# Optimization experiments

Measured on AMD Instinct MI355X. Metric: run time of the kernel, lower is better.

Reference implementation:

```python
import jax, jax.numpy as jnp
import numpy as np

B, T, V, E, H = 32, 128, 32000, 512, 1024
START = 1


def setup_inputs() -> dict:
    key = jax.random.key(0)
    ks = jax.random.split(key, 16)
    s = 0.02
    inp = {
        'h0': jax.random.normal(ks[0], (B, H), jnp.float32),
        'c0': jax.random.normal(ks[1], (B, H), jnp.float32),
        'h1': jax.random.normal(ks[2], (B, H), jnp.float32),
        'c1': jax.random.normal(ks[3], (B, H), jnp.float32),
        'h2': jax.random.normal(ks[4], (B, H), jnp.float32),
        'c2': jax.random.normal(ks[5], (B, H), jnp.float32),
        'h3': jax.random.normal(ks[6], (B, H), jnp.float32),
        'c3': jax.random.normal(ks[7], (B, H), jnp.float32),
        'emb': jax.random.normal(ks[8], (V, E), jnp.float32) * s,
        'Wx0': jax.random.normal(ks[9], (E, 4 * H), jnp.float32) * s,
        'Wh0': jax.random.normal(ks[10], (H, 4 * H), jnp.float32) * s,
        'b0': jnp.zeros((4 * H,), jnp.float32),
        'Wx1': jax.random.normal(ks[11], (H, 4 * H), jnp.float32) * s,
        'Wh1': jax.random.normal(ks[12], (H, 4 * H), jnp.float32) * s,
        'b1': jnp.zeros((4 * H,), jnp.float32),
        'Wx2': jax.random.normal(ks[13], (H, 4 * H), jnp.float32) * s,
        'Wh2': jax.random.normal(ks[14], (H, 4 * H), jnp.float32) * s,
        'b2': jnp.zeros((4 * H,), jnp.float32),
        'Wx3': jax.random.normal(ks[15], (H, 4 * H), jnp.float32) * s,
        'Wh3': jax.random.normal(jax.random.fold_in(key, 99), (H, 4 * H), jnp.float32) * s,
        'b3': jnp.zeros((4 * H,), jnp.float32),
        'fcW': jax.random.normal(jax.random.fold_in(key, 100), (H, V), jnp.float32) * s,
        'fcb': jnp.zeros((V,), jnp.float32),
        'target_length': T,
    }
    return inp


def _lstm_cell(x, h, c, Wx, Wh, b):
    # Keras gate order: i, f, c(candidate), o
    z = x @ Wx + h @ Wh + b  # [B, 4H]
    i, f, g, o = jnp.split(z, 4, axis=-1)
    i = jax.nn.sigmoid(i)
    f = jax.nn.sigmoid(f)
    g = jnp.tanh(g)
    o = jax.nn.sigmoid(o)
    c_new = f * c + i * g
    h_new = o * jnp.tanh(c_new)
    return h_new, c_new


def reference(h0, c0, h1, c1, h2, c2, h3, c3, emb,
              Wx0, Wh0, b0, Wx1, Wh1, b1, Wx2, Wh2, b2, Wx3, Wh3, b3,
              fcW, fcb, target_length):
    n_batch = h0.shape[0]
    tok0 = jnp.full((n_batch,), START, dtype=jnp.int32)

    def step(carry, _):
        tok, h0, c0, h1, c1, h2, c2, h3, c3 = carry
        x = emb[tok]  # [B, E]
        h0, c0 = _lstm_cell(x, h0, c0, Wx0, Wh0, b0)
        h1, c1 = _lstm_cell(h0, h1, c1, Wx1, Wh1, b1)
        h2, c2 = _lstm_cell(h1, h2, c2, Wx2, Wh2, b2)
        h3, c3 = _lstm_cell(h2, h3, c3, Wx3, Wh3, b3)
        logits = h3 @ fcW + fcb  # [B, V]
        tok = jnp.argmax(logits, axis=1).astype(jnp.int32)
        return (tok, h0, c0, h1, c1, h2, c2, h3, c3), (logits, tok)

    carry0 = (tok0, h0, c0, h1, c1, h2, c2, h3, c3)
    _, (logits_seq, ids_seq) = jax.lax.scan(step, carry0, None, length=target_length)
    outputs_prob = jnp.transpose(logits_seq, (1, 0, 2))  # [B, T, V]
    outputs = jnp.transpose(ids_seq, (1, 0))             # [B, T]
    return outputs_prob, outputs
```

## Files before the change

kernel.cpp:

```cpp
#include <hip/hip_runtime.h>
#include <stdint.h>

#define NBLK 256
#define NTHR 1024

typedef _Float16 f16;
typedef _Float16 f16x8 __attribute__((ext_vector_type(8)));
typedef float f32x4 __attribute__((ext_vector_type(4)));
typedef unsigned long long u64;


__device__ __forceinline__ void split2(float w, f16& hi, f16& lo) {
  f16 h = (__builtin_fabsf(w) < 6.104e-05f) ? (f16)0.0f : (f16)w;
  hi = h;
  lo = (f16)((w - (float)h) * 2048.0f);
}

__device__ __forceinline__ void split3(float w, f16& h, f16& l, f16& m) {
  const float hf = (__builtin_fabsf(w) < 6.104e-05f) ? 0.0f : (float)(f16)w;
  h = (f16)hf;
  const float r1s = (w - hf) * 2048.0f;
  const float lf = (__builtin_fabsf(r1s) < 6.104e-05f) ? 0.0f : (float)(f16)r1s;
  l = (f16)lf;
  const float r2s = (r1s - lf) * 2048.0f;
  m = (__builtin_fabsf(r2s) < 6.104e-05f) ? (f16)0.0f : (f16)r2s;
}

__device__ __forceinline__ float sig32(float z) {
  const float e32 = (float)exp(-(double)z);
  return 1.0f / __fadd_rn(1.0f, e32);
}
__device__ __forceinline__ float tanh32f(float z) { return (float)tanh((double)z); }

__device__ __forceinline__ u64 packvc(float v, unsigned col) {
  unsigned u = __float_as_uint(v);
  u = (u & 0x80000000u) ? ~u : (u | 0x80000000u);
  return ((u64)u << 32) | (u64)(0xFFFFFFFFu - col);
}
__device__ __forceinline__ u64 umax64(u64 a, u64 b) { return a > b ? a : b; }

__device__ __forceinline__ size_t faddr(int k, int row) {
  return (size_t)(((k >> 5) * 2 + (row >> 4)) * 512 +
                  (16 * ((k >> 3) & 3) + (row & 15)) * 8 + (k & 7));
}


struct MainP {
  const float* emb;
  const float* bias[4];
  const float* fcb;
  const float* hini[4];
  const float* cini[4];
  const f16* WfH[4];
  const f16* WfL[4];
  const f16* fcH;
  const f16* fcLc;
  const float* shat;
  f16* axh[5];
  f16* axl[5];
  f16* axm[5];
  u64* top;
  unsigned* bar;
  float* out;
};


__device__ __forceinline__ void grid_bar2(unsigned* bar, int blk) {
  __syncthreads();
  if (threadIdx.x == 0) {
    const int g = blk >> 5;
    unsigned* gcnt = bar + g * 32;
    unsigned* ggen = bar + g * 32 + 16;
    unsigned* tcnt = bar + 512;
    unsigned* tgen = bar + 528;
    unsigned gg = __hip_atomic_load(ggen, __ATOMIC_RELAXED, __HIP_MEMORY_SCOPE_AGENT);
    unsigned prev = __hip_atomic_fetch_add(gcnt, 1u, __ATOMIC_ACQ_REL, __HIP_MEMORY_SCOPE_AGENT);
    if (prev == 31u) {
      unsigned tg = __hip_atomic_load(tgen, __ATOMIC_RELAXED, __HIP_MEMORY_SCOPE_AGENT);
      unsigned p2 = __hip_atomic_fetch_add(tcnt, 1u, __ATOMIC_ACQ_REL, __HIP_MEMORY_SCOPE_AGENT);
      if (p2 == 7u) {
        __hip_atomic_store(tcnt, 0u, __ATOMIC_RELAXED, __HIP_MEMORY_SCOPE_AGENT);
        __hip_atomic_store(tgen, tg + 1u, __ATOMIC_RELEASE, __HIP_MEMORY_SCOPE_AGENT);
      } else {
        while (__hip_atomic_load(tgen, __ATOMIC_RELAXED, __HIP_MEMORY_SCOPE_AGENT) == tg)
          __builtin_amdgcn_s_sleep(1);
        __builtin_amdgcn_fence(__ATOMIC_ACQUIRE, "agent");
      }
      __hip_atomic_store(gcnt, 0u, __ATOMIC_RELAXED, __HIP_MEMORY_SCOPE_AGENT);
      __hip_atomic_store(ggen, gg + 1u, __ATOMIC_RELEASE, __HIP_MEMORY_SCOPE_AGENT);
    } else {
      while (__hip_atomic_load(ggen, __ATOMIC_RELAXED, __HIP_MEMORY_SCOPE_AGENT) == gg)
        __builtin_amdgcn_s_sleep(2);
      __builtin_amdgcn_fence(__ATOMIC_ACQUIRE, "agent");
    }
  }
  __syncthreads();
}


__global__ __launch_bounds__(256) void prep_lstm(const float* Wx, const float* Wh,
                                                 int Kx, int CH, f16* dh, f16* dl) {
  const int id = blockIdx.x * 256 + threadIdx.x;
  const int lane = id & 63;
  const int cw = id >> 6;
  const int tile = cw / CH;
  if (tile >= 256) return;
  const int chunk = cw - tile * CH;
  const int n16 = lane & 15, qq = lane >> 4;
  const int col = 1024 * (n16 >> 2) + 4 * tile + (n16 & 3);
  const int kb = chunk * 32 + 8 * qq;
  f16x8 hv, lv;
#pragma unroll
  for (int e = 0; e < 8; ++e) {
    const int k = kb + e;
    const float wv = (k < Kx) ? Wx[(size_t)k * 4096 + col] : Wh[(size_t)(k - Kx) * 4096 + col];
    f16 h, l;
    split2(wv, h, l);
    hv[e] = h; lv[e] = l;
  }
  const size_t d = ((size_t)cw * 64 + lane) * 8;
  *(f16x8*)(dh + d) = hv;
  *(f16x8*)(dl + d) = lv;
}

__global__ __launch_bounds__(256) void prep_fc(const float* fcW, f16* dh) {
  const int id = blockIdx.x * 256 + threadIdx.x;
  const int lane = id & 63;
  const int cw = id >> 6;
  const int chunk = cw & 31;
  const int stb = cw >> 5;
  const int st = stb & 7, blk = stb >> 3;
  if (blk >= 256) return;
  const int n16 = lane & 15, qq = lane >> 4;
  int cl = st * 16 + n16;
  if (cl > 124) cl = 124;
  const int col = 125 * blk + cl;
  const int kb = chunk * 32 + 8 * qq;
  f16x8 hv;
#pragma unroll
  for (int e = 0; e < 8; ++e) {
    const float wv = fcW[(size_t)(kb + e) * 32000 + col];
    f16 h, l;
    split2(wv, h, l);
    hv[e] = h; (void)l;
  }
  const size_t d = ((size_t)cw * 64 + lane) * 8;
  *(f16x8*)(dh + d) = hv;
}

__global__ __launch_bounds__(256) void prep_fclT(const float* fcW, f16* fcLc) {
  const int col0 = blockIdx.x * 64;
  const int tid = threadIdx.x;
  __shared__ float lds[64][65];
  for (int pass = 0; pass < 16; ++pass) {
    const int kbase = pass * 64;
#pragma unroll
    for (int rr = 0; rr < 16; ++rr) {
      const int kk = rr * 4 + (tid >> 6);
      lds[kk][tid & 63] = fcW[(size_t)(kbase + kk) * 32000 + col0 + (tid & 63)];
    }
    __syncthreads();
    {
      const int col = tid >> 2, qr = tid & 3;
      f16x8 v0, v1;
#pragma unroll
      for (int i = 0; i < 8; ++i) {
        f16 h, l;
        split2(lds[qr * 16 + i][col], h, l);
        v0[i] = l;
      }
#pragma unroll
      for (int i = 0; i < 8; ++i) {
        f16 h, l;
        split2(lds[qr * 16 + 8 + i][col], h, l);
        v1[i] = l;
      }
      const size_t d = (size_t)(col0 + col) * 1024 + kbase + qr * 16;
      *(f16x8*)(fcLc + d) = v0;
      *(f16x8*)(fcLc + d + 8) = v1;
    }
    __syncthreads();
  }
}

__global__ __launch_bounds__(256) void prep_shat(const float* fcW, float* shat) {
  const int id = blockIdx.x * 256 + threadIdx.x;
  if (id >= 256 * 1024) return;
  const int blk = id >> 10, k = id & 1023;
  const float* src = fcW + (size_t)k * 32000 + 125 * blk;
  float s = 0.f;
  for (int c = 0; c < 125; ++c) {
    f16 h, l;
    split2(src[c], h, l);
    s = fmaxf(s, __builtin_fabsf((float)l));
  }
  shat[id] = s;
}

__global__ void ws_sentinel(float* out) {
  if (blockIdx.x == 0 && threadIdx.x == 0) out[0] = 1.0e9f;
}


__global__ __launch_bounds__(NTHR, 4) void lstm_main(MainP p) {
  const int blk = blockIdx.x;
  const int tid = threadIdx.x;
  const int lane = tid & 63;
  const int w = tid >> 6;
  const int q = lane >> 4;
  const int n16 = lane & 15;

  __shared__ float zpart[16][2][32][16];
  __shared__ float fcpart[2][32][128];
  __shared__ float zred[32][16];
  __shared__ float rmaxs[32][16];
  __shared__ float epart[32][16];
  __shared__ float rowmax[32];
  __shared__ float erow[32];
  __shared__ float cst[4][32][4];
  __shared__ f16 hs_h[32][4], hs_l[32][4], hs_m[32][4];
  __shared__ int tokS[32];
  __shared__ u64 redu[32][16];
  __shared__ u64 redu2[32];
  __shared__ int wl[4000];
  __shared__ unsigned cand[32][4];
  __shared__ int wcount;

  if (tid < 512) {
    const int i = tid;
    const int l = i >> 7, b = (i >> 2) & 31, j = i & 3;
    cst[l][b][j] = p.cini[l][b * 1024 + 4 * blk + j];
    f16 hh, ll, mm;
    split3(p.hini[l][b * 1024 + 4 * blk + j], hh, ll, mm);
    const int kp = (l == 0) ? (4 * blk + j) : (1024 + 4 * blk + j);
    const size_t a = faddr(kp, b);
    p.axh[l][a] = hh;
    p.axl[l][a] = ll;
    p.axm[l][a] = mm;
  }
  grid_bar2(p.bar, blk);

  auto layer_tail = [&](int l, const float* bias, f16* dh, f16* dl, f16* dm) {
    __syncthreads();
    if (tid < 512) {
      const int row = tid >> 4, c = tid & 15;
      double A = 0.0, B = 0.0;
#pragma unroll
      for (int w2 = 0; w2 < 16; ++w2) {
        A += (double)zpart[w2][0][row][c];
        B += (double)zpart[w2][1][row][c];
      }
      zred[row][c] = __fadd_rn(__fadd_rn((float)A, (float)B),
                               bias[1024 * (c >> 2) + 4 * blk + (c & 3)]);
    }
    __syncthreads();
    if (tid < 128) {
      const int b = tid >> 2, j = tid & 3;
      const float zi = zred[b][j], zf = zred[b][4 + j], zg = zred[b][8 + j], zo = zred[b][12 + j];
      const float i_ = sig32(zi);
      const float f_ = sig32(zf);
      const float g_ = tanh32f(zg);
      const float o_ = sig32(zo);
      const float c_ = __fadd_rn(__fmul_rn(f_, cst[l][b][j]), __fmul_rn(i_, g_));
      cst[l][b][j] = c_;
      const float h_ = __fmul_rn(o_, tanh32f(c_));
      f16 hh, ll, mm;
      split3(h_, hh, ll, mm);
      hs_h[b][j] = hh; hs_l[b][j] = ll; hs_m[b][j] = mm;
      const size_t a = faddr(4 * blk + j, b);
      dh[a] = hh; dl[a] = ll; dm[a] = mm;
    }
  };

  for (int t = 0; t < 128; ++t) {
    if (t == 0) {
      if (tid < 32) tokS[tid] = 1;
    } else {
      if (tid < 512) {
        const int row = tid >> 4, seg = tid & 15;
        const u64* tr = p.top + row * 256 + seg * 16;
        u64 m = 0;
#pragma unroll
        for (int e = 0; e < 16; ++e) m = umax64(m, tr[e]);
        redu[row][seg] = m;
      }
      __syncthreads();
      if (tid < 32) {
        u64 mm = redu[tid][0];
#pragma unroll
        for (int s2 = 1; s2 < 16; ++s2) mm = umax64(mm, redu[tid][s2]);
        const int tok = (int)(0xFFFFFFFFu - (unsigned)(mm & 0xFFFFFFFFull));
        tokS[tid] = tok;
        if (blk == tid)
          p.out[(size_t)32 * 128 * 32000 + (size_t)tid * 128 + (t - 1)] = (float)tok;
      }
    }
    __syncthreads();

    {
      double zdA0[4] = {0,0,0,0}, zdA1[4] = {0,0,0,0};
      double zdB0[4] = {0,0,0,0}, zdB1[4] = {0,0,0,0};
      const f32x4 zz = {0.f, 0.f, 0.f, 0.f};
      f16x8 WB[6];
#pragma unroll
      for (int sl = 0; sl < 3; ++sl) {
        const size_t wo = ((size_t)(blk * 48 + w * 3 + sl) * 64 + lane) * 8;
        WB[sl * 2] = *(const f16x8*)(p.WfH[0] + wo);
        WB[sl * 2 + 1] = *(const f16x8*)(p.WfL[0] + wo);
      }
#pragma unroll
      for (int sl = 0; sl < 3; ++sl) {
        const int chunk = w * 3 + sl;
        const int k0 = chunk * 32 + 8 * q;
        const f16x8 bh = WB[sl * 2];
        const f16x8 bl = WB[sl * 2 + 1];
        f16x8 ah0, al0, am0, ah1, al1, am1;
        if (chunk < 16) {
          {
            const float* ep = p.emb + (size_t)tokS[n16] * 512 + k0;
            const float4 v0 = *(const float4*)ep;
            const float4 v1 = *(const float4*)(ep + 4);
            const float vv[8] = {v0.x, v0.y, v0.z, v0.w, v1.x, v1.y, v1.z, v1.w};
#pragma unroll
            for (int e = 0; e < 8; ++e) { f16 a,b,c; split3(vv[e],a,b,c); ah0[e]=a; al0[e]=b; am0[e]=c; }
          }
          {
            const float* ep = p.emb + (size_t)tokS[16 + n16] * 512 + k0;
            const float4 v0 = *(const float4*)ep;
            const float4 v1 = *(const float4*)(ep + 4);
            const float vv[8] = {v0.x, v0.y, v0.z, v0.w, v1.x, v1.y, v1.z, v1.w};
#pragma unroll
            for (int e = 0; e < 8; ++e) { f16 a,b,c; split3(vv[e],a,b,c); ah1[e]=a; al1[e]=b; am1[e]=c; }
          }
        } else {
          const int cs = chunk - 16;
          const size_t b0 = (size_t)(cs * 2) * 512 + lane * 8;
          ah0 = *(const f16x8*)(p.axh[0] + b0);
          al0 = *(const f16x8*)(p.axl[0] + b0);
          am0 = *(const f16x8*)(p.axm[0] + b0);
          ah1 = *(const f16x8*)(p.axh[0] + b0 + 512);
          al1 = *(const f16x8*)(p.axl[0] + b0 + 512);
          am1 = *(const f16x8*)(p.axm[0] + b0 + 512);
        }
        f32x4 t00 = __builtin_amdgcn_mfma_f32_16x16x32_f16(ah0, bh, zz, 0, 0, 0);
        f32x4 t10 = __builtin_amdgcn_mfma_f32_16x16x32_f16(ah0, bl, zz, 0, 0, 0);
        t10 = __builtin_amdgcn_mfma_f32_16x16x32_f16(al0, bh, t10, 0, 0, 0);
        f32x4 t20 = __builtin_amdgcn_mfma_f32_16x16x32_f16(al0, bl, zz, 0, 0, 0);
        t20 = __builtin_amdgcn_mfma_f32_16x16x32_f16(am0, bh, t20, 0, 0, 0);
        f32x4 t01 = __builtin_amdgcn_mfma_f32_16x16x32_f16(ah1, bh, zz, 0, 0, 0);
        f32x4 t11 = __builtin_amdgcn_mfma_f32_16x16x32_f16(ah1, bl, zz, 0, 0, 0);
        t11 = __builtin_amdgcn_mfma_f32_16x16x32_f16(al1, bh, t11, 0, 0, 0);
        f32x4 t21 = __builtin_amdgcn_mfma_f32_16x16x32_f16(al1, bl, zz, 0, 0, 0);
        t21 = __builtin_amdgcn_mfma_f32_16x16x32_f16(am1, bh, t21, 0, 0, 0);
        if (chunk < 16) {
#pragma unroll
          for (int r = 0; r < 4; ++r) {
            zdA0[r] += (double)t00[r] + (double)t10[r] * 0x1p-11 + (double)t20[r] * 0x1p-22;
            zdA1[r] += (double)t01[r] + (double)t11[r] * 0x1p-11 + (double)t21[r] * 0x1p-22;
          }
        } else {
#pragma unroll
          for (int r = 0; r < 4; ++r) {
            zdB0[r] += (double)t00[r] + (double)t10[r] * 0x1p-11 + (double)t20[r] * 0x1p-22;
            zdB1[r] += (double)t01[r] + (double)t11[r] * 0x1p-11 + (double)t21[r] * 0x1p-22;
          }
        }
      }
#pragma unroll
      for (int r = 0; r < 4; ++r) {
        zpart[w][0][4 * q + r][n16] = (float)zdA0[r];
        zpart[w][0][16 + 4 * q + r][n16] = (float)zdA1[r];
        zpart[w][1][4 * q + r][n16] = (float)zdB0[r];
        zpart[w][1][16 + 4 * q + r][n16] = (float)zdB1[r];
      }
    }
    layer_tail(0, p.bias[0], p.axh[1], p.axl[1], p.axm[1]);
    grid_bar2(p.bar, blk);

    for (int l = 1; l < 4; ++l) {
      if (tid < 128) {
        const int b = tid >> 2, j = tid & 3;
        const int kp = (l == 1) ? (4 * blk + j) : (1024 + 4 * blk + j);
        const size_t a = faddr(kp, b);
        p.axh[l - 1][a] = hs_h[b][j];
        p.axl[l - 1][a] = hs_l[b][j];
        p.axm[l - 1][a] = hs_m[b][j];
      }
      {
        double zdA0[4] = {0,0,0,0}, zdA1[4] = {0,0,0,0};
        double zdB0[4] = {0,0,0,0}, zdB1[4] = {0,0,0,0};
        const f16* WH = p.WfH[l];
        const f16* WL = p.WfL[l];
        const f16* axh_ = p.axh[l];
        const f16* axl_ = p.axl[l];
        const f16* axm_ = p.axm[l];
        const f32x4 zz = {0.f, 0.f, 0.f, 0.f};
        f16x8 WB[8];
#pragma unroll
        for (int sl = 0; sl < 4; ++sl) {
          const size_t wo = ((size_t)(blk * 64 + w * 4 + sl) * 64 + lane) * 8;
          WB[sl * 2] = *(const f16x8*)(WH + wo);
          WB[sl * 2 + 1] = *(const f16x8*)(WL + wo);
        }
#pragma unroll
        for (int sl = 0; sl < 4; ++sl) {
          const int chunk = w * 4 + sl;
          const f16x8 bh = WB[sl * 2];
          const f16x8 bl = WB[sl * 2 + 1];
          const size_t b0 = (size_t)(chunk * 2) * 512 + lane * 8;
          const f16x8 ah0 = *(const f16x8*)(axh_ + b0);
          const f16x8 al0 = *(const f16x8*)(axl_ + b0);
          const f16x8 am0 = *(const f16x8*)(axm_ + b0);
          const f16x8 ah1 = *(const f16x8*)(axh_ + b0 + 512);
          const f16x8 al1 = *(const f16x8*)(axl_ + b0 + 512);
          const f16x8 am1 = *(const f16x8*)(axm_ + b0 + 512);
          f32x4 t00 = __builtin_amdgcn_mfma_f32_16x16x32_f16(ah0, bh, zz, 0, 0, 0);
          f32x4 t10 = __builtin_amdgcn_mfma_f32_16x16x32_f16(ah0, bl, zz, 0, 0, 0);
          t10 = __builtin_amdgcn_mfma_f32_16x16x32_f16(al0, bh, t10, 0, 0, 0);
          f32x4 t20 = __builtin_amdgcn_mfma_f32_16x16x32_f16(al0, bl, zz, 0, 0, 0);
          t20 = __builtin_amdgcn_mfma_f32_16x16x32_f16(am0, bh, t20, 0, 0, 0);
          f32x4 t01 = __builtin_amdgcn_mfma_f32_16x16x32_f16(ah1, bh, zz, 0, 0, 0);
          f32x4 t11 = __builtin_amdgcn_mfma_f32_16x16x32_f16(ah1, bl, zz, 0, 0, 0);
          t11 = __builtin_amdgcn_mfma_f32_16x16x32_f16(al1, bh, t11, 0, 0, 0);
          f32x4 t21 = __builtin_amdgcn_mfma_f32_16x16x32_f16(al1, bl, zz, 0, 0, 0);
          t21 = __builtin_amdgcn_mfma_f32_16x16x32_f16(am1, bh, t21, 0, 0, 0);
          if (chunk < 32) {
#pragma unroll
            for (int r = 0; r < 4; ++r) {
              zdA0[r] += (double)t00[r] + (double)t10[r] * 0x1p-11 + (double)t20[r] * 0x1p-22;
              zdA1[r] += (double)t01[r] + (double)t11[r] * 0x1p-11 + (double)t21[r] * 0x1p-22;
            }
          } else {
#pragma unroll
            for (int r = 0; r < 4; ++r) {
              zdB0[r] += (double)t00[r] + (double)t10[r] * 0x1p-11 + (double)t20[r] * 0x1p-22;
              zdB1[r] += (double)t01[r] + (double)t11[r] * 0x1p-11 + (double)t21[r] * 0x1p-22;
            }
          }
        }
#pragma unroll
        for (int r = 0; r < 4; ++r) {
          zpart[w][0][4 * q + r][n16] = (float)zdA0[r];
          zpart[w][0][16 + 4 * q + r][n16] = (float)zdA1[r];
          zpart[w][1][4 * q + r][n16] = (float)zdB0[r];
          zpart[w][1][16 + 4 * q + r][n16] = (float)zdB1[r];
        }
      }
      if (l < 3) layer_tail(l, p.bias[l], p.axh[l + 1], p.axl[l + 1], p.axm[l + 1]);
      else       layer_tail(l, p.bias[l], p.axh[4], p.axl[4], p.axm[4]);
      grid_bar2(p.bar, blk);
    }

    if (tid < 128) {
      const int b = tid >> 2, j = tid & 3;
      const size_t a = faddr(1024 + 4 * blk + j, b);
      p.axh[3][a] = hs_h[b][j];
      p.axl[3][a] = hs_l[b][j];
      p.axm[3][a] = hs_m[b][j];
    }
    if (tid < 32) redu2[tid] = 0ull;
    if (tid < 128) cand[tid >> 2][tid & 3] = 0u;
    if (tid == 0) wcount = 0;
    {
      const int kh = w & 1;
      const int st = w >> 1;
      double Ld0[4] = {0,0,0,0}, Ld1[4] = {0,0,0,0};
      const f32x4 zz = {0.f, 0.f, 0.f, 0.f};
      f16x8 FB[8];
#pragma unroll
      for (int g = 0; g < 2; ++g) {
#pragma unroll
        for (int i = 0; i < 8; ++i) {
          const int chunk = kh * 16 + g * 8 + i;
          FB[i] = *(const f16x8*)(p.fcH + (((size_t)(blk * 8 + st) * 32 + chunk) * 64 + lane) * 8);
        }
#pragma unroll
        for (int i = 0; i < 8; ++i) {
          const int chunk = kh * 16 + g * 8 + i;
          const size_t ab = (size_t)(chunk * 2) * 512 + lane * 8;
          const f16x8 ah0 = *(const f16x8*)(p.axh[4] + ab);
          const f16x8 al0 = *(const f16x8*)(p.axl[4] + ab);
          const f16x8 am0 = *(const f16x8*)(p.axm[4] + ab);
          const f16x8 ah1 = *(const f16x8*)(p.axh[4] + ab + 512);
          const f16x8 al1 = *(const f16x8*)(p.axl[4] + ab + 512);
          const f16x8 am1 = *(const f16x8*)(p.axm[4] + ab + 512);
          const f16x8 bh = FB[i];
          f32x4 t00 = __builtin_amdgcn_mfma_f32_16x16x32_f16(ah0, bh, zz, 0, 0, 0);
          f32x4 t10 = __builtin_amdgcn_mfma_f32_16x16x32_f16(al0, bh, zz, 0, 0, 0);
          f32x4 t20 = __builtin_amdgcn_mfma_f32_16x16x32_f16(am0, bh, zz, 0, 0, 0);
          f32x4 t01 = __builtin_amdgcn_mfma_f32_16x16x32_f16(ah1, bh, zz, 0, 0, 0);
          f32x4 t11 = __builtin_amdgcn_mfma_f32_16x16x32_f16(al1, bh, zz, 0, 0, 0);
          f32x4 t21 = __builtin_amdgcn_mfma_f32_16x16x32_f16(am1, bh, zz, 0, 0, 0);
#pragma unroll
          for (int r = 0; r < 4; ++r) {
            Ld0[r] += (double)t00[r] + (double)t10[r] * 0x1p-11 + (double)t20[r] * 0x1p-22;
            Ld1[r] += (double)t01[r] + (double)t11[r] * 0x1p-11 + (double)t21[r] * 0x1p-22;
          }
        }
      }
#pragma unroll
      for (int r = 0; r < 4; ++r) {
        fcpart[kh][4 * q + r][st * 16 + n16] = (float)Ld0[r];
        fcpart[kh][16 + 4 * q + r][st * 16 + n16] = (float)Ld1[r];
      }
    }
    __syncthreads();
    if (tid < 512) {
      const int row = tid >> 4, cg = tid & 15;
#pragma unroll
      for (int cc = 0; cc < 8; ++cc) {
        const int c = cg * 8 + cc;
        if (c < 125) {
          const double hiD = (double)fcpart[0][row][c] + (double)fcpart[1][row][c];
          const float pre = (float)hiD;
          const float z = __fadd_rn(pre, p.fcb[125 * blk + c]);
          fcpart[0][row][c] = z;
          fcpart[1][row][c] = pre;
        }
      }
    } else {
      const int idx = tid - 512;
      const int row = idx >> 4, seg = idx & 15;
      const float* sh = p.shat + (size_t)blk * 1024 + seg * 64;
      float s = 0.f;
#pragma unroll 8
      for (int i = 0; i < 64; ++i) {
        const float av = __builtin_fabsf((float)p.axh[4][faddr(seg * 64 + i, row)]) + 1e-5f;
        s += av * sh[i];
      }
      epart[row][seg] = s;
    }
    __syncthreads();
    if (tid < 512) {
      const int row = tid >> 4, cg = tid & 15;
      float m = -3.4e38f;
#pragma unroll
      for (int cc = 0; cc < 8; ++cc) {
        const int c = cg * 8 + cc;
        if (c < 125) m = fmaxf(m, fcpart[0][row][c]);
      }
      rmaxs[row][cg] = m;
    }
    __syncthreads();
    if (tid < 32) {
      float m = rmaxs[tid][0];
      float e = epart[tid][0];
#pragma unroll
      for (int s2 = 1; s2 < 16; ++s2) { m = fmaxf(m, rmaxs[tid][s2]); e += epart[tid][s2]; }
      rowmax[tid] = m;
      erow[tid] = 2.0f * (e * (1.0f / 2048.0f)) * 1.02f + 2e-5f;
    }
    __syncthreads();
    for (int idx = tid; idx < 32 * 128; idx += NTHR) {
      const int row = idx >> 7, c = idx & 127;
      if (c < 125) {
        if (fcpart[0][row][c] >= rowmax[row] - erow[row]) {
          const int pos = atomicAdd(&wcount, 1);
          wl[pos] = (row << 8) | c;
          atomicOr(&cand[row][c >> 5], 1u << (c & 31));
        }
      }
    }
    __syncthreads();
    if (w < 8) {
      const int row = tid >> 4, cg = tid & 15;
      float* orow = p.out + (size_t)row * (128 * 32000) + (size_t)t * 32000 + 125 * blk;
#pragma unroll
      for (int cc = 0; cc < 8; ++cc) {
        const int c = cg * 8 + cc;
        if (c < 125 && !((cand[row][c >> 5] >> (c & 31)) & 1u))
          __builtin_nontemporal_store(fcpart[0][row][c], orow + c);
      }
    } else {
      const int wcnt = wcount;
      for (int i = w - 8; i < wcnt; i += 8) {
        const int ent = wl[i];
        const int row = ent >> 8, cl = ent & 255;
        const int kb = lane * 16;
        const f16x8 A0h = *(const f16x8*)(p.axh[4] + faddr(kb, row));
        const f16x8 A0l = *(const f16x8*)(p.axl[4] + faddr(kb, row));
        const f16x8 A0m = *(const f16x8*)(p.axm[4] + faddr(kb, row));
        const f16x8 A1h = *(const f16x8*)(p.axh[4] + faddr(kb + 8, row));
        const f16x8 A1l = *(const f16x8*)(p.axl[4] + faddr(kb + 8, row));
        const f16x8 A1m = *(const f16x8*)(p.axm[4] + faddr(kb + 8, row));
        const f16* Lc = p.fcLc + (size_t)(125 * blk + cl) * 1024 + kb;
        const f16x8 L0 = *(const f16x8*)(Lc);
        const f16x8 L1 = *(const f16x8*)(Lc + 8);
        double d = 0.0;
#pragma unroll
        for (int e = 0; e < 8; ++e) {
          const double a0 = (double)A0h[e] + (double)A0l[e] * 0x1p-11 + (double)A0m[e] * 0x1p-22;
          const double a1 = (double)A1h[e] + (double)A1l[e] * 0x1p-11 + (double)A1m[e] * 0x1p-22;
          d += a0 * (double)L0[e] + a1 * (double)L1[e];
        }
#pragma unroll
        for (int m2 = 32; m2 >= 1; m2 >>= 1) d += __shfl_xor(d, m2, 64);
        if (lane == 0) {
          const float zr = __fadd_rn((float)((double)fcpart[1][row][cl] + d * 0x1p-11),
                                     p.fcb[125 * blk + cl]);
          atomicMax(&redu2[row], packvc(zr, (unsigned)(125 * blk + cl)));
          p.out[(size_t)row * (128 * 32000) + (size_t)t * 32000 + 125 * blk + cl] = zr;
        }
      }
    }
    __syncthreads();
    if (tid < 32) p.top[tid * 256 + blk] = redu2[tid];
    grid_bar2(p.bar, blk);
  }

  if (blk < 32) {
    if (tid < 16) {
      const u64* tr = p.top + blk * 256 + tid * 16;
      u64 m = 0;
#pragma unroll
      for (int e = 0; e < 16; ++e) m = umax64(m, tr[e]);
      redu[0][tid] = m;
    }
    __syncthreads();
    if (tid == 0) {
      u64 mm = redu[0][0];
#pragma unroll
      for (int s2 = 1; s2 < 16; ++s2) mm = umax64(mm, redu[0][s2]);
      p.out[(size_t)32 * 128 * 32000 + (size_t)blk * 128 + 127] =
          (float)(0xFFFFFFFFu - (unsigned)(mm & 0xFFFFFFFFull));
    }
  }
}


extern "C" void kernel_launch(void* const* d_in, const int* in_sizes, int n_in,
                              void* d_out, int out_size, void* d_ws, size_t ws_size,
                              hipStream_t stream) {
  (void)in_sizes; (void)n_in; (void)out_size;
  const float* hini[4] = {(const float*)d_in[0], (const float*)d_in[2], (const float*)d_in[4], (const float*)d_in[6]};
  const float* cini[4] = {(const float*)d_in[1], (const float*)d_in[3], (const float*)d_in[5], (const float*)d_in[7]};
  const float* emb = (const float*)d_in[8];
  const float* Wx[4] = {(const float*)d_in[9], (const float*)d_in[12], (const float*)d_in[15], (const float*)d_in[18]};
  const float* Wh[4] = {(const float*)d_in[10], (const float*)d_in[13], (const float*)d_in[16], (const float*)d_in[19]};
  const float* bias[4] = {(const float*)d_in[11], (const float*)d_in[14], (const float*)d_in[17], (const float*)d_in[20]};
  const float* fcW = (const float*)d_in[21];
  const float* fcb = (const float*)d_in[22];

  char* ws = (char*)d_ws;
  size_t off = 0;
  auto take = [&](size_t bytes) -> char* {
    char* r = ws + off;
    off += (bytes + 255) & ~(size_t)255;
    return r;
  };
  f16* WfH[4]; f16* WfL[4];
  WfH[0] = (f16*)take((size_t)256 * 48 * 64 * 8 * 2);
  WfL[0] = (f16*)take((size_t)256 * 48 * 64 * 8 * 2);
  for (int l = 1; l < 4; ++l) {
    WfH[l] = (f16*)take((size_t)256 * 64 * 64 * 8 * 2);
    WfL[l] = (f16*)take((size_t)256 * 64 * 64 * 8 * 2);
  }
  f16* fcH = (f16*)take((size_t)256 * 8 * 32 * 64 * 8 * 2);
  f16* fcLc = (f16*)take((size_t)32000 * 1024 * 2);
  float* shat = (float*)take((size_t)256 * 1024 * 4);
  f16* axh[5]; f16* axl[5]; f16* axm[5];
  const int axK[5] = {1024, 2048, 2048, 2048, 1024};
  for (int l = 0; l < 5; ++l) {
    axh[l] = (f16*)take((size_t)axK[l] * 32 * 2);
    axl[l] = (f16*)take((size_t)axK[l] * 32 * 2);
    axm[l] = (f16*)take((size_t)axK[l] * 32 * 2);
  }
  u64* top = (u64*)take((size_t)32 * 256 * 8);
  unsigned* bar = (unsigned*)take(2560);

  if (off > ws_size) {
    hipLaunchKernelGGL(ws_sentinel, dim3(1), dim3(1), 0, stream, (float*)d_out);
    return;
  }

  hipMemsetAsync(bar, 0, 2560, stream);
  hipLaunchKernelGGL(prep_lstm, dim3(256 * 48 * 64 / 256), dim3(256), 0, stream,
                     Wx[0], Wh[0], 512, 48, WfH[0], WfL[0]);
  for (int l = 1; l < 4; ++l)
    hipLaunchKernelGGL(prep_lstm, dim3(256 * 64 * 64 / 256), dim3(256), 0, stream,
                       Wx[l], Wh[l], 1024, 64, WfH[l], WfL[l]);
  hipLaunchKernelGGL(prep_fc, dim3(256 * 8 * 32 * 64 / 256), dim3(256), 0, stream,
                     fcW, fcH);
  hipLaunchKernelGGL(prep_fclT, dim3(500), dim3(256), 0, stream, fcW, fcLc);
  hipLaunchKernelGGL(prep_shat, dim3(1024), dim3(256), 0, stream, fcW, shat);

  MainP mp;
  mp.emb = emb;
  for (int l = 0; l < 4; ++l) {
    mp.bias[l] = bias[l]; mp.hini[l] = hini[l]; mp.cini[l] = cini[l];
    mp.WfH[l] = WfH[l]; mp.WfL[l] = WfL[l];
  }
  mp.fcb = fcb; mp.fcH = fcH; mp.fcLc = fcLc; mp.shat = shat;
  for (int l = 0; l < 5; ++l) { mp.axh[l] = axh[l]; mp.axl[l] = axl[l]; mp.axm[l] = axm[l]; }
  mp.top = top; mp.bar = bar; mp.out = (float*)d_out;

  void* args[] = {&mp};
  hipLaunchCooperativeKernel((void*)lstm_main, dim3(NBLK), dim3(NTHR), args, 0, stream);
}
```

Before: 31.37 ms.

## Halve block size and keep layer 1-2 weights resident in registers

Cuts the persistent kernel from 1024 to 512 threads per block, so each wave covers twice as many K-chunks. With the spare register budget, the split-fp16 weights for LSTM layers 1 and 2 are loaded into registers once before the time loop instead of being re-read every step. The FC stage no longer splits K across two halves, which removes the double-precision combine. Fewer waves means less latency hiding and more serial work per wave, and the large register arrays risk spilling.

```diff
diff --git a/kernel.cpp b/kernel.cpp
--- a/kernel.cpp
+++ b/kernel.cpp
@@ -2,7 +2,7 @@
 #include <stdint.h>
 
 #define NBLK 256
-#define NTHR 1024
+#define NTHR 512
 
 typedef _Float16 f16;
 typedef _Float16 f16x8 __attribute__((ext_vector_type(8)));
@@ -202,7 +202,7 @@
 }
 
 
-__global__ __launch_bounds__(NTHR, 4) void lstm_main(MainP p) {
+__global__ __launch_bounds__(NTHR, 2) void lstm_main(MainP p) {
   const int blk = blockIdx.x;
   const int tid = threadIdx.x;
   const int lane = tid & 63;
@@ -210,7 +210,7 @@
   const int q = lane >> 4;
   const int n16 = lane & 15;
 
-  __shared__ float zpart[16][2][32][16];
+  __shared__ float zpart[8][2][32][16];
   __shared__ float fcpart[2][32][128];
   __shared__ float zred[32][16];
   __shared__ float rmaxs[32][16];
@@ -226,7 +226,17 @@
   __shared__ unsigned cand[32][4];
   __shared__ int wcount;
 
-  if (tid < 512) {
+  f16x8 w1h[8], w1l[8], w2h[8], w2l[8];
+#pragma unroll
+  for (int sl = 0; sl < 8; ++sl) {
+    const size_t wo = ((size_t)(blk * 64 + w * 8 + sl) * 64 + lane) * 8;
+    w1h[sl] = *(const f16x8*)(p.WfH[1] + wo);
+    w1l[sl] = *(const f16x8*)(p.WfL[1] + wo);
+    w2h[sl] = *(const f16x8*)(p.WfH[2] + wo);
+    w2l[sl] = *(const f16x8*)(p.WfL[2] + wo);
+  }
+
+  {
     const int i = tid;
     const int l = i >> 7, b = (i >> 2) & 31, j = i & 3;
     cst[l][b][j] = p.cini[l][b * 1024 + 4 * blk + j];
@@ -242,11 +252,11 @@
 
   auto layer_tail = [&](int l, const float* bias, f16* dh, f16* dl, f16* dm) {
     __syncthreads();
-    if (tid < 512) {
+    {
       const int row = tid >> 4, c = tid & 15;
       double A = 0.0, B = 0.0;
 #pragma unroll
-      for (int w2 = 0; w2 < 16; ++w2) {
+      for (int w2 = 0; w2 < 8; ++w2) {
         A += (double)zpart[w2][0][row][c];
         B += (double)zpart[w2][1][row][c];
       }
@@ -272,11 +282,61 @@
     }
   };
 
+  auto lstm_layer_regs = [&](const f16x8 (&WH)[8], const f16x8 (&WL)[8],
+                             const f16* axh_, const f16* axl_, const f16* axm_) {
+    double zdA0[4] = {0,0,0,0}, zdA1[4] = {0,0,0,0};
+    double zdB0[4] = {0,0,0,0}, zdB1[4] = {0,0,0,0};
+    const f32x4 zz = {0.f, 0.f, 0.f, 0.f};
+#pragma unroll
+    for (int sl = 0; sl < 8; ++sl) {
+      const int chunk = w * 8 + sl;
+      const f16x8 bh = WH[sl];
+      const f16x8 bl = WL[sl];
+      const size_t b0 = (size_t)(chunk * 2) * 512 + lane * 8;
+      const f16x8 ah0 = *(const f16x8*)(axh_ + b0);
+      const f16x8 al0 = *(const f16x8*)(axl_ + b0);
+      const f16x8 am0 = *(const f16x8*)(axm_ + b0);
+      const f16x8 ah1 = *(const f16x8*)(axh_ + b0 + 512);
+      const f16x8 al1 = *(const f16x8*)(axl_ + b0 + 512);
+      const f16x8 am1 = *(const f16x8*)(axm_ + b0 + 512);
+      f32x4 t00 = __builtin_amdgcn_mfma_f32_16x16x32_f16(ah0, bh, zz, 0, 0, 0);
+      f32x4 t10 = __builtin_amdgcn_mfma_f32_16x16x32_f16(ah0, bl, zz, 0, 0, 0);
+      t10 = __builtin_amdgcn_mfma_f32_16x16x32_f16(al0, bh, t10, 0, 0, 0);
+      f32x4 t20 = __builtin_amdgcn_mfma_f32_16x16x32_f16(al0, bl, zz, 0, 0, 0);
+      t20 = __builtin_amdgcn_mfma_f32_16x16x32_f16(am0, bh, t20, 0, 0, 0);
+      f32x4 t01 = __builtin_amdgcn_mfma_f32_16x16x32_f16(ah1, bh, zz, 0, 0, 0);
+      f32x4 t11 = __builtin_amdgcn_mfma_f32_16x16x32_f16(ah1, bl, zz, 0, 0, 0);
+      t11 = __builtin_amdgcn_mfma_f32_16x16x32_f16(al1, bh, t11, 0, 0, 0);
+      f32x4 t21 = __builtin_amdgcn_mfma_f32_16x16x32_f16(al1, bl, zz, 0, 0, 0);
+      t21 = __builtin_amdgcn_mfma_f32_16x16x32_f16(am1, bh, t21, 0, 0, 0);
+      if (w < 4) {
+#pragma unroll
+        for (int r = 0; r < 4; ++r) {
+          zdA0[r] += (double)t00[r] + (double)t10[r] * 0x1p-11 + (double)t20[r] * 0x1p-22;
+          zdA1[r] += (double)t01[r] + (double)t11[r] * 0x1p-11 + (double)t21[r] * 0x1p-22;
+        }
+      } else {
+#pragma unroll
+        for (int r = 0; r < 4; ++r) {
+          zdB0[r] += (double)t00[r] + (double)t10[r] * 0x1p-11 + (double)t20[r] * 0x1p-22;
+          zdB1[r] += (double)t01[r] + (double)t11[r] * 0x1p-11 + (double)t21[r] * 0x1p-22;
+        }
+      }
+    }
+#pragma unroll
+    for (int r = 0; r < 4; ++r) {
+      zpart[w][0][4 * q + r][n16] = (float)zdA0[r];
+      zpart[w][0][16 + 4 * q + r][n16] = (float)zdA1[r];
+      zpart[w][1][4 * q + r][n16] = (float)zdB0[r];
+      zpart[w][1][16 + 4 * q + r][n16] = (float)zdB1[r];
+    }
+  };
+
   for (int t = 0; t < 128; ++t) {
     if (t == 0) {
       if (tid < 32) tokS[tid] = 1;
     } else {
-      if (tid < 512) {
+      {
         const int row = tid >> 4, seg = tid & 15;
         const u64* tr = p.top + row * 256 + seg * 16;
         u64 m = 0;
@@ -301,68 +361,71 @@
       double zdA0[4] = {0,0,0,0}, zdA1[4] = {0,0,0,0};
       double zdB0[4] = {0,0,0,0}, zdB1[4] = {0,0,0,0};
       const f32x4 zz = {0.f, 0.f, 0.f, 0.f};
-      f16x8 WB[6];
-#pragma unroll
-      for (int sl = 0; sl < 3; ++sl) {
-        const size_t wo = ((size_t)(blk * 48 + w * 3 + sl) * 64 + lane) * 8;
-        WB[sl * 2] = *(const f16x8*)(p.WfH[0] + wo);
-        WB[sl * 2 + 1] = *(const f16x8*)(p.WfL[0] + wo);
-      }
-#pragma unroll
-      for (int sl = 0; sl < 3; ++sl) {
-        const int chunk = w * 3 + sl;
-        const int k0 = chunk * 32 + 8 * q;
-        const f16x8 bh = WB[sl * 2];
-        const f16x8 bl = WB[sl * 2 + 1];
-        f16x8 ah0, al0, am0, ah1, al1, am1;
-        if (chunk < 16) {
-          {
-            const float* ep = p.emb + (size_t)tokS[n16] * 512 + k0;
-            const float4 v0 = *(const float4*)ep;
-            const float4 v1 = *(const float4*)(ep + 4);
-            const float vv[8] = {v0.x, v0.y, v0.z, v0.w, v1.x, v1.y, v1.z, v1.w};
-#pragma unroll
-            for (int e = 0; e < 8; ++e) { f16 a,b,c; split3(vv[e],a,b,c); ah0[e]=a; al0[e]=b; am0[e]=c; }
+      for (int gg = 0; gg < 2; ++gg) {
+        f16x8 WB[6];
+#pragma unroll
+        for (int s2 = 0; s2 < 3; ++s2) {
+          const int chunk = w * 6 + gg * 3 + s2;
+          const size_t wo = ((size_t)(blk * 48 + chunk) * 64 + lane) * 8;
+          WB[s2 * 2] = *(const f16x8*)(p.WfH[0] + wo);
+          WB[s2 * 2 + 1] = *(const f16x8*)(p.WfL[0] + wo);
+        }
+#pragma unroll
+        for (int s2 = 0; s2 < 3; ++s2) {
+          const int chunk = w * 6 + gg * 3 + s2;
+          const int k0 = chunk * 32 + 8 * q;
+          const f16x8 bh = WB[s2 * 2];
+          const f16x8 bl = WB[s2 * 2 + 1];
+          f16x8 ah0, al0, am0, ah1, al1, am1;
+          if (chunk < 16) {
+            {
+              const float* ep = p.emb + (size_t)tokS[n16] * 512 + k0;
+              const float4 v0 = *(const float4*)ep;
+              const float4 v1 = *(const float4*)(ep + 4);
+              const float vv[8] = {v0.x, v0.y, v0.z, v0.w, v1.x, v1.y, v1.z, v1.w};
+#pragma unroll
+              for (int e = 0; e < 8; ++e) { f16 a,b,c; split3(vv[e],a,b,c); ah0[e]=a; al0[e]=b; am0[e]=c; }
+            }
+            {
+              const float* ep = p.emb + (size_t)tokS[16 + n16] * 512 + k0;
+              const float4 v0 = *(const float4*)ep;
+              const float4 v1 = *(const float4*)(ep + 4);
+              const float vv[8] = {v0.x, v0.y, v0.z, v0.w, v1.x, v1.y, v1.z, v1.w};
+#pragma unroll
+              for (int e = 0; e < 8; ++e) { f16 a,b,c; split3(vv[e],a,b,c); ah1[e]=a; al1[e]=b; am1[e]=c; }
+            }
+          } else {
+            const int cs = chunk - 16;
+            const size_t b0 = (size_t)(cs * 2) * 512 + lane * 8;
+            ah0 = *(const f16x8*)(p.axh[0] + b0);
+            al0 = *(const f16x8*)(p.axl[0] + b0);
+            am0 = *(const f16x8*)(p.axm[0] + b0);
+            ah1 = *(const f16x8*)(p.axh[0] + b0 + 512);
+            al1 = *(const f16x8*)(p.axl[0] + b0 + 512);
+            am1 = *(const f16x8*)(p.axm[0] + b0 + 512);
           }
-          {
-            const float* ep = p.emb + (size_t)tokS[16 + n16] * 512 + k0;
-            const float4 v0 = *(const float4*)ep;
-            const float4 v1 = *(const float4*)(ep + 4);
-            const float vv[8] = {v0.x, v0.y, v0.z, v0.w, v1.x, v1.y, v1.z, v1.w};
-#pragma unroll
-            for (int e = 0; e < 8; ++e) { f16 a,b,c; split3(vv[e],a,b,c); ah1[e]=a; al1[e]=b; am1[e]=c; }
-          }
-        } else {
-          const int cs = chunk - 16;
-          const size_t b0 = (size_t)(cs * 2) * 512 + lane * 8;
-          ah0 = *(const f16x8*)(p.axh[0] + b0);
-          al0 = *(const f16x8*)(p.axl[0] + b0);
-          am0 = *(const f16x8*)(p.axm[0] + b0);
-          ah1 = *(const f16x8*)(p.axh[0] + b0 + 512);
-          al1 = *(const f16x8*)(p.axl[0] + b0 + 512);
-          am1 = *(const f16x8*)(p.axm[0] + b0 + 512);
-        }
-        f32x4 t00 = __builtin_amdgcn_mfma_f32_16x16x32_f16(ah0, bh, zz, 0, 0, 0);
-        f32x4 t10 = __builtin_amdgcn_mfma_f32_16x16x32_f16(ah0, bl, zz, 0, 0, 0);
-        t10 = __builtin_amdgcn_mfma_f32_16x16x32_f16(al0, bh, t10, 0, 0, 0);
-        f32x4 t20 = __builtin_amdgcn_mfma_f32_16x16x32_f16(al0, bl, zz, 0, 0, 0);
-        t20 = __builtin_amdgcn_mfma_f32_16x16x32_f16(am0, bh, t20, 0, 0, 0);
-        f32x4 t01 = __builtin_amdgcn_mfma_f32_16x16x32_f16(ah1, bh, zz, 0, 0, 0);
-        f32x4 t11 = __builtin_amdgcn_mfma_f32_16x16x32_f16(ah1, bl, zz, 0, 0, 0);
-        t11 = __builtin_amdgcn_mfma_f32_16x16x32_f16(al1, bh, t11, 0, 0, 0);
-        f32x4 t21 = __builtin_amdgcn_mfma_f32_16x16x32_f16(al1, bl, zz, 0, 0, 0);
-        t21 = __builtin_amdgcn_mfma_f32_16x16x32_f16(am1, bh, t21, 0, 0, 0);
-        if (chunk < 16) {
-#pragma unroll
-          for (int r = 0; r < 4; ++r) {
-            zdA0[r] += (double)t00[r] + (double)t10[r] * 0x1p-11 + (double)t20[r] * 0x1p-22;
-            zdA1[r] += (double)t01[r] + (double)t11[r] * 0x1p-11 + (double)t21[r] * 0x1p-22;
-          }
-        } else {
-#pragma unroll
-          for (int r = 0; r < 4; ++r) {
-            zdB0[r] += (double)t00[r] + (double)t10[r] * 0x1p-11 + (double)t20[r] * 0x1p-22;
-            zdB1[r] += (double)t01[r] + (double)t11[r] * 0x1p-11 + (double)t21[r] * 0x1p-22;
+          f32x4 t00 = __builtin_amdgcn_mfma_f32_16x16x32_f16(ah0, bh, zz, 0, 0, 0);
+          f32x4 t10 = __builtin_amdgcn_mfma_f32_16x16x32_f16(ah0, bl, zz, 0, 0, 0);
+          t10 = __builtin_amdgcn_mfma_f32_16x16x32_f16(al0, bh, t10, 0, 0, 0);
+          f32x4 t20 = __builtin_amdgcn_mfma_f32_16x16x32_f16(al0, bl, zz, 0, 0, 0);
+          t20 = __builtin_amdgcn_mfma_f32_16x16x32_f16(am0, bh, t20, 0, 0, 0);
+          f32x4 t01 = __builtin_amdgcn_mfma_f32_16x16x32_f16(ah1, bh, zz, 0, 0, 0);
+          f32x4 t11 = __builtin_amdgcn_mfma_f32_16x16x32_f16(ah1, bl, zz, 0, 0, 0);
+          t11 = __builtin_amdgcn_mfma_f32_16x16x32_f16(al1, bh, t11, 0, 0, 0);
+          f32x4 t21 = __builtin_amdgcn_mfma_f32_16x16x32_f16(al1, bl, zz, 0, 0, 0);
+          t21 = __builtin_amdgcn_mfma_f32_16x16x32_f16(am1, bh, t21, 0, 0, 0);
+          if (chunk < 16) {
+#pragma unroll
+            for (int r = 0; r < 4; ++r) {
+              zdA0[r] += (double)t00[r] + (double)t10[r] * 0x1p-11 + (double)t20[r] * 0x1p-22;
+              zdA1[r] += (double)t01[r] + (double)t11[r] * 0x1p-11 + (double)t21[r] * 0x1p-22;
+            }
+          } else {
+#pragma unroll
+            for (int r = 0; r < 4; ++r) {
+              zdB0[r] += (double)t00[r] + (double)t10[r] * 0x1p-11 + (double)t20[r] * 0x1p-22;
+              zdB1[r] += (double)t01[r] + (double)t11[r] * 0x1p-11 + (double)t21[r] * 0x1p-22;
+            }
           }
         }
       }
@@ -377,36 +440,56 @@
     layer_tail(0, p.bias[0], p.axh[1], p.axl[1], p.axm[1]);
     grid_bar2(p.bar, blk);
 
-    for (int l = 1; l < 4; ++l) {
-      if (tid < 128) {
-        const int b = tid >> 2, j = tid & 3;
-        const int kp = (l == 1) ? (4 * blk + j) : (1024 + 4 * blk + j);
-        const size_t a = faddr(kp, b);
-        p.axh[l - 1][a] = hs_h[b][j];
-        p.axl[l - 1][a] = hs_l[b][j];
-        p.axm[l - 1][a] = hs_m[b][j];
-      }
-      {
-        double zdA0[4] = {0,0,0,0}, zdA1[4] = {0,0,0,0};
-        double zdB0[4] = {0,0,0,0}, zdB1[4] = {0,0,0,0};
-        const f16* WH = p.WfH[l];
-        const f16* WL = p.WfL[l];
-        const f16* axh_ = p.axh[l];
-        const f16* axl_ = p.axl[l];
-        const f16* axm_ = p.axm[l];
-        const f32x4 zz = {0.f, 0.f, 0.f, 0.f};
+    if (tid < 128) {
+      const int b = tid >> 2, j = tid & 3;
+      const size_t a = faddr(4 * blk + j, b);
+      p.axh[0][a] = hs_h[b][j];
+      p.axl[0][a] = hs_l[b][j];
+      p.axm[0][a] = hs_m[b][j];
+    }
+    lstm_layer_regs(w1h, w1l, p.axh[1], p.axl[1], p.axm[1]);
+    layer_tail(1, p.bias[1], p.axh[2], p.axl[2], p.axm[2]);
+    grid_bar2(p.bar, blk);
+
+    if (tid < 128) {
+      const int b = tid >> 2, j = tid & 3;
+      const size_t a = faddr(1024 + 4 * blk + j, b);
+      p.axh[1][a] = hs_h[b][j];
+      p.axl[1][a] = hs_l[b][j];
+      p.axm[1][a] = hs_m[b][j];
+    }
+    lstm_layer_regs(w2h, w2l, p.axh[2], p.axl[2], p.axm[2]);
+    layer_tail(2, p.bias[2], p.axh[3], p.axl[3], p.axm[3]);
+    grid_bar2(p.bar, blk);
+
+    if (tid < 128) {
+      const int b = tid >> 2, j = tid & 3;
+      const size_t a = faddr(1024 + 4 * blk + j, b);
+      p.axh[2][a] = hs_h[b][j];
+      p.axl[2][a] = hs_l[b][j];
+      p.axm[2][a] = hs_m[b][j];
+    }
+    {
+      double zdA0[4] = {0,0,0,0}, zdA1[4] = {0,0,0,0};
+      double zdB0[4] = {0,0,0,0}, zdB1[4] = {0,0,0,0};
+      const f16* axh_ = p.axh[3];
+      const f16* axl_ = p.axl[3];
+      const f16* axm_ = p.axm[3];
+      const f32x4 zz = {0.f, 0.f, 0.f, 0.f};
+      for (int gg = 0; gg < 2; ++gg) {
         f16x8 WB[8];
 #pragma unroll
-        for (int sl = 0; sl < 4; ++sl) {
-          const size_t wo = ((size_t)(blk * 64 + w * 4 + sl) * 64 + lane) * 8;
-          WB[sl * 2] = *(const f16x8*)(WH + wo);
-          WB[sl * 2 + 1] = *(const f16x8*)(WL + wo);
-        }
-#pragma unroll
-        for (int sl = 0; sl < 4; ++sl) {
-          const int chunk = w * 4 + sl;
-          const f16x8 bh = WB[sl * 2];
-          const f16x8 bl = WB[sl * 2 + 1];
+        for (int s2 = 0; s2 < 4; ++s2) {
+          const int chunk = w * 8 + gg * 4 + s2;
+          const size_t wo = ((size_t)(blk * 64 + chunk) * 64 + lane) * 8;
+          WB[s2 * 2] = *(const f16x8*)(p.WfH[3] + wo);
+          WB[s2 * 2 + 1] = *(const f16x8*)(p.WfL[3] + wo);
+        }
+#pragma unroll
+        for (int s2 = 0; s2 < 4; ++s2) {
+          const int chunk = w * 8 + gg * 4 + s2;
+          const f16x8 bh = WB[s2 * 2];
+          const f16x8 bl = WB[s2 * 2 + 1];
           const size_t b0 = (size_t)(chunk * 2) * 512 + lane * 8;
           const f16x8 ah0 = *(const f16x8*)(axh_ + b0);
           const f16x8 al0 = *(const f16x8*)(axl_ + b0);
@@ -424,7 +507,7 @@
           t11 = __builtin_amdgcn_mfma_f32_16x16x32_f16(al1, bh, t11, 0, 0, 0);
           f32x4 t21 = __builtin_amdgcn_mfma_f32_16x16x32_f16(al1, bl, zz, 0, 0, 0);
           t21 = __builtin_amdgcn_mfma_f32_16x16x32_f16(am1, bh, t21, 0, 0, 0);
-          if (chunk < 32) {
+          if (w < 4) {
 #pragma unroll
             for (int r = 0; r < 4; ++r) {
               zdA0[r] += (double)t00[r] + (double)t10[r] * 0x1p-11 + (double)t20[r] * 0x1p-22;
@@ -438,18 +521,17 @@
             }
           }
         }
-#pragma unroll
-        for (int r = 0; r < 4; ++r) {
-          zpart[w][0][4 * q + r][n16] = (float)zdA0[r];
-          zpart[w][0][16 + 4 * q + r][n16] = (float)zdA1[r];
-          zpart[w][1][4 * q + r][n16] = (float)zdB0[r];
-          zpart[w][1][16 + 4 * q + r][n16] = (float)zdB1[r];
-        }
-      }
-      if (l < 3) layer_tail(l, p.bias[l], p.axh[l + 1], p.axl[l + 1], p.axm[l + 1]);
-      else       layer_tail(l, p.bias[l], p.axh[4], p.axl[4], p.axm[4]);
-      grid_bar2(p.bar, blk);
-    }
+      }
+#pragma unroll
+      for (int r = 0; r < 4; ++r) {
+        zpart[w][0][4 * q + r][n16] = (float)zdA0[r];
+        zpart[w][0][16 + 4 * q + r][n16] = (float)zdA1[r];
+        zpart[w][1][4 * q + r][n16] = (float)zdB0[r];
+        zpart[w][1][16 + 4 * q + r][n16] = (float)zdB1[r];
+      }
+    }
+    layer_tail(3, p.bias[3], p.axh[4], p.axl[4], p.axm[4]);
+    grid_bar2(p.bar, blk);
 
     if (tid < 128) {
       const int b = tid >> 2, j = tid & 3;
@@ -462,21 +544,19 @@
     if (tid < 128) cand[tid >> 2][tid & 3] = 0u;
     if (tid == 0) wcount = 0;
     {
-      const int kh = w & 1;
-      const int st = w >> 1;
+      const int st = w;
       double Ld0[4] = {0,0,0,0}, Ld1[4] = {0,0,0,0};
       const f32x4 zz = {0.f, 0.f, 0.f, 0.f};
-      f16x8 FB[8];
-#pragma unroll
-      for (int g = 0; g < 2; ++g) {
+      for (int g = 0; g < 4; ++g) {
+        f16x8 FB[8];
 #pragma unroll
         for (int i = 0; i < 8; ++i) {
-          const int chunk = kh * 16 + g * 8 + i;
+          const int chunk = g * 8 + i;
           FB[i] = *(const f16x8*)(p.fcH + (((size_t)(blk * 8 + st) * 32 + chunk) * 64 + lane) * 8);
         }
 #pragma unroll
         for (int i = 0; i < 8; ++i) {
-          const int chunk = kh * 16 + g * 8 + i;
+          const int chunk = g * 8 + i;
           const size_t ab = (size_t)(chunk * 2) * 512 + lane * 8;
           const f16x8 ah0 = *(const f16x8*)(p.axh[4] + ab);
           const f16x8 al0 = *(const f16x8*)(p.axl[4] + ab);
@@ -500,27 +580,22 @@
       }
 #pragma unroll
       for (int r = 0; r < 4; ++r) {
-        fcpart[kh][4 * q + r][st * 16 + n16] = (float)Ld0[r];
-        fcpart[kh][16 + 4 * q + r][st * 16 + n16] = (float)Ld1[r];
-      }
-    }
-    __syncthreads();
-    if (tid < 512) {
+        fcpart[1][4 * q + r][st * 16 + n16] = (float)Ld0[r];
+        fcpart[1][16 + 4 * q + r][st * 16 + n16] = (float)Ld1[r];
+      }
+    }
+    __syncthreads();
+    {
       const int row = tid >> 4, cg = tid & 15;
 #pragma unroll
       for (int cc = 0; cc < 8; ++cc) {
         const int c = cg * 8 + cc;
         if (c < 125) {
-          const double hiD = (double)fcpart[0][row][c] + (double)fcpart[1][row][c];
-          const float pre = (float)hiD;
-          const float z = __fadd_rn(pre, p.fcb[125 * blk + c]);
-          fcpart[0][row][c] = z;
-          fcpart[1][row][c] = pre;
-        }
-      }
-    } else {
-      const int idx = tid - 512;
-      const int row = idx >> 4, seg = idx & 15;
+          const float pre = fcpart[1][row][c];
+          fcpart[0][row][c] = __fadd_rn(pre, p.fcb[125 * blk + c]);
+        }
+      }
+      const int seg = cg;
       const float* sh = p.shat + (size_t)blk * 1024 + seg * 64;
       float s = 0.f;
 #pragma unroll 8
@@ -531,7 +606,7 @@
       epart[row][seg] = s;
     }
     __syncthreads();
-    if (tid < 512) {
+    {
       const int row = tid >> 4, cg = tid & 15;
       float m = -3.4e38f;
 #pragma unroll
@@ -562,18 +637,18 @@
       }
     }
     __syncthreads();
-    if (w < 8) {
-      const int row = tid >> 4, cg = tid & 15;
+    if (w < 4) {
+      const int row = tid >> 3, cg = tid & 7;
       float* orow = p.out + (size_t)row * (128 * 32000) + (size_t)t * 32000 + 125 * blk;
 #pragma unroll
-      for (int cc = 0; cc < 8; ++cc) {
-        const int c = cg * 8 + cc;
+      for (int cc = 0; cc < 16; ++cc) {
+        const int c = cg * 16 + cc;
         if (c < 125 && !((cand[row][c >> 5] >> (c & 31)) & 1u))
           __builtin_nontemporal_store(fcpart[0][row][c], orow + c);
       }
     } else {
       const int wcnt = wcount;
-      for (int i = w - 8; i < wcnt; i += 8) {
+      for (int i = w - 4; i < wcnt; i += 4) {
         const int ent = wl[i];
         const int row = ent >> 8, cl = ent & 255;
         const int kb = lane * 16;
```

After: 30.34 ms. -3.3%, faster.
